# Kernel optimization log

Hardware: AMD Instinct MI355X
Metric: run time of the kernel (lower is better)

The kernel has to match this reference:

```python
import jax, jax.numpy as jnp
import numpy as np

B, T, V, E, D, F = 128, 64, 10000, 512, 512, 2048


def setup_inputs() -> dict:
    key = jax.random.key(0)
    ks = iter(jax.random.split(key, 40))
    def nrm(shape, s=0.02):
        return (jax.random.normal(next(ks), shape, jnp.float32) * s)
    inp = {
        "image_vectors": jax.random.normal(next(ks), (B, F), jnp.float32),
        "captions_ix": jax.random.randint(next(ks), (B, T), 0, V),
        "emb": nrm((V, E)),
        "W_init_h1": nrm((D, F)), "b_init_h1": jnp.zeros((D,), jnp.float32),
        "W_init_c1": nrm((D, F)), "b_init_c1": jnp.zeros((D,), jnp.float32),
        "W_init_h2": nrm((D, F)), "b_init_h2": jnp.zeros((D,), jnp.float32),
        "W_init_c2": nrm((D, F)), "b_init_c2": jnp.zeros((D,), jnp.float32),
        "W_ih1": nrm((4 * D, E)), "W_hh1": nrm((4 * D, D)), "b1": jnp.zeros((4 * D,), jnp.float32),
        "W_ih2": nrm((4 * D, 2 * D)), "W_hh2": nrm((4 * D, D)), "b2": jnp.zeros((4 * D,), jnp.float32),
        "Wv1": nrm((D, D)), "bv1": jnp.zeros((D,), jnp.float32),
        "Wo1": nrm((D, D)), "bo1": jnp.zeros((D,), jnp.float32),
        "Wv2": nrm((D, D)), "bv2": jnp.zeros((D,), jnp.float32),
        "Wo2": nrm((D, D)), "bo2": jnp.zeros((D,), jnp.float32),
        "W_logits": nrm((V, 3 * D)), "b_logits": jnp.zeros((V,), jnp.float32),
    }
    return inp


def _lstm(x, h0, c0, W_ih, W_hh, b):
    # x: [B,T,Din] -> hidden states [B,T,D]; PyTorch gate order (i,f,g,o), b = b_ih + b_hh.
    xp = jnp.einsum('btd,gd->btg', x, W_ih) + b  # precompute input projections
    def step(carry, xt):
        h, c = carry
        gates = xt + h @ W_hh.T
        i, f, g, o = jnp.split(gates, 4, axis=-1)
        c = jax.nn.sigmoid(f) * c + jax.nn.sigmoid(i) * jnp.tanh(g)
        h = jax.nn.sigmoid(o) * jnp.tanh(c)
        return (h, c), h
    _, hs = jax.lax.scan(step, (h0, c0), jnp.swapaxes(xp, 0, 1))
    return jnp.swapaxes(hs, 0, 1)


def reference(image_vectors, captions_ix, emb,
              W_init_h1, b_init_h1, W_init_c1, b_init_c1,
              W_init_h2, b_init_h2, W_init_c2, b_init_c2,
              W_ih1, W_hh1, b1, W_ih2, W_hh2, b2,
              Wv1, bv1, Wo1, bo1, Wv2, bv2, Wo2, bo2,
              W_logits, b_logits):
    h1 = image_vectors @ W_init_h1.T + b_init_h1
    c1 = image_vectors @ W_init_c1.T + b_init_c1
    h2 = image_vectors @ W_init_h2.T + b_init_h2
    c2 = image_vectors @ W_init_c2.T + b_init_c2
    x = emb[captions_ix]  # [B,T,E] (dropout p=0 -> identity)
    h1s = _lstm(x, h1, c1, W_ih1, W_hh1, b1)  # [B,T,D]; LSTM output == hidden state
    # MHA with key=value of length 1: softmax over one key is exactly 1, so the
    # output is out_proj(v_proj(key)) independent of the (growing prefix) query.
    attn1 = (h1s @ Wv1.T + bv1) @ Wo1.T + bo1  # [B,T,D]
    h2s = _lstm(jnp.concatenate([h1s, attn1], axis=-1), h2, c2, W_ih2, W_hh2, b2)
    attn2 = (h2s @ Wv2.T + bv2) @ Wo2.T + bo2
    out = jnp.concatenate([h2s, attn1, attn2], axis=-1)  # [B,T,3D]
    return out @ W_logits.T + b_logits  # [B,T,V]
```

## Files before the change

kernel.cpp:

```cpp
#include <hip/hip_runtime.h>
#include <stdint.h>

#define DEV __device__ __forceinline__

typedef short bf16x8 __attribute__((ext_vector_type(8)));
typedef float f32x4 __attribute__((ext_vector_type(4)));

DEV unsigned short f2bf(float f) {
  union { float f; uint32_t u; } v; v.f = f;
  return (unsigned short)((v.u + 0x7fffu + ((v.u >> 16) & 1u)) >> 16);
}
DEV float bf2f(unsigned short u) {
  union { uint32_t u; float f; } v; v.u = (uint32_t)u << 16; return v.f;
}

DEV float fsig(float x) { return 1.f / (1.f + __expf(-x)); }
DEV float ftanh(float x) { float e = __expf(2.f * x); return 1.f - 2.f / (e + 1.f); }

DEV void gload16(const void* g, void* lds) {
  __builtin_amdgcn_global_load_lds(
      (const __attribute__((address_space(1))) int*)(uintptr_t)g,
      (__attribute__((address_space(3))) int*)(uintptr_t)lds, 16, 0, 0);
}

template <int MODE>
__global__ __launch_bounds__(256) void gemm_nt(
    const unsigned short* __restrict__ A, int lda,
    const unsigned short* __restrict__ B, int ldb,
    void* __restrict__ P0, void* __restrict__ P1,
    void* __restrict__ P2, void* __restrict__ P3,
    int ldc, int ldc2,
    const float* __restrict__ bias,
    int K, int Nreal)
{
  __shared__ alignas(16) unsigned short Asm[128 * 32];
  __shared__ alignas(16) unsigned short Bsm[128 * 32];
  const int tid = threadIdx.x;
  const int wave = tid >> 6, lane = tid & 63;

  const int gx = gridDim.x;
  const int lin = blockIdx.y * gx + blockIdx.x;
  const int nwg = gx * gridDim.y;
  const int q = nwg >> 3, r = nwg & 7;
  const int xcd = lin & 7, i2 = lin >> 3;
  const int wg = (xcd < r ? xcd * (q + 1) : r * (q + 1) + (xcd - r) * q) + i2;
  const int m0 = (wg % gx) * 128, n0 = (wg / gx) * 128;

  const int wr = wave >> 1, wc = wave & 1;
  f32x4 acc[4][4] = {};

  const int q0 = tid, q1 = tid + 256;
  const unsigned short* Ag0 = A + (size_t)(m0 + (q0 >> 2)) * lda + (q0 & 3) * 8;
  const unsigned short* Ag1 = A + (size_t)(m0 + (q1 >> 2)) * lda + (q1 & 3) * 8;
  const unsigned short* Bg0 = B + (size_t)(n0 + (q0 >> 2)) * ldb + (q0 & 3) * 8;
  const unsigned short* Bg1 = B + (size_t)(n0 + (q1 >> 2)) * ldb + (q1 & 3) * 8;
  char* As0 = (char*)Asm + wave * 1024;  char* As1 = As0 + 4096;
  char* Bs0 = (char*)Bsm + wave * 1024;  char* Bs1 = Bs0 + 4096;

  const int ra = wr * 64 + (lane & 15);
  const int rb = wc * 64 + (lane & 15);
  const int kb = (lane >> 4) * 16;

  for (int k0 = 0; k0 < K; k0 += 32) {
    gload16(Ag0 + k0, As0);
    gload16(Ag1 + k0, As1);
    gload16(Bg0 + k0, Bs0);
    gload16(Bg1 + k0, Bs1);
    __syncthreads();
    bf16x8 af[4], bfr[4];
#pragma unroll
    for (int i = 0; i < 4; ++i)
      af[i] = *(const bf16x8*)((const char*)Asm + (ra + i * 16) * 64 + kb);
#pragma unroll
    for (int i = 0; i < 4; ++i)
      bfr[i] = *(const bf16x8*)((const char*)Bsm + (rb + i * 16) * 64 + kb);
#pragma unroll
    for (int mi = 0; mi < 4; ++mi)
#pragma unroll
      for (int ni = 0; ni < 4; ++ni)
        acc[mi][ni] = __builtin_amdgcn_mfma_f32_16x16x32_bf16(af[mi], bfr[ni], acc[mi][ni], 0, 0, 0);
    __syncthreads();
  }

  const int row0 = m0 + wr * 64 + (lane >> 4) * 4;
  const int col0 = n0 + wc * 64 + (lane & 15);

  if constexpr (MODE == 2) {
#pragma unroll
    for (int mi = 0; mi < 4; ++mi) {
      const int rowb = row0 + mi * 16;
      const int dd = rowb >> 2;
      const float4 b4 = *(const float4*)&bias[rowb];
#pragma unroll
      for (int ni = 0; ni < 4; ++ni) {
        const int col = col0 + ni * 16;
        const int tt = col & 63, bb = col >> 6;
        float4 v;
        v.x = acc[mi][ni][0] + b4.x;
        v.y = acc[mi][ni][1] + b4.y;
        v.z = acc[mi][ni][2] + b4.z;
        v.w = acc[mi][ni][3] + b4.w;
        const int wgid = (bb >> 4) * 16 + (dd >> 5);
        const int ww = (dd >> 3) & 3, mi2 = (dd >> 2) & 1, ln = (dd & 3) * 16 + (bb & 15);
        ((float4*)P0)[((((size_t)tt * 128 + wgid) * 4 + ww) * 2 + mi2) * 64 + ln] = v;
      }
    }
    return;
  }

#pragma unroll
  for (int mi = 0; mi < 4; ++mi) {
#pragma unroll
    for (int ni = 0; ni < 4; ++ni) {
      const int col = col0 + ni * 16;
      if (col >= Nreal) continue;
      const float bs = bias ? bias[col] : 0.f;
#pragma unroll
      for (int rr = 0; rr < 4; ++rr) {
        const int row = row0 + mi * 16 + rr;
        const float v = acc[mi][ni][rr] + bs;
        if constexpr (MODE == 1) {
          ((unsigned short*)P0)[(size_t)row * ldc + col] = f2bf(v);
          if (P1) ((unsigned short*)P1)[(size_t)row * ldc2 + col] = f2bf(v);
        } else if constexpr (MODE == 4) {
          const unsigned short ad = ((const unsigned short*)P1)[(size_t)row * ldc2 + col];
          ((unsigned short*)P0)[(size_t)row * ldc + col] = f2bf(v + bf2f(ad));
        } else {
          const int seg = col >> 9, cc = col & 511;
          if (seg == 0)      ((unsigned short*)P0)[(size_t)row * 512 + cc] = f2bf(v);
          else if (seg == 1) ((float*)P1)[(size_t)row * 512 + cc] = v;
          else if (seg == 2) ((unsigned short*)P2)[(size_t)row * 512 + cc] = f2bf(v);
          else               ((float*)P3)[(size_t)row * 512 + cc] = v;
        }
      }
    }
  }
}

__global__ __launch_bounds__(512, 2) void gemm256(
    const unsigned short* __restrict__ A, int lda,
    const unsigned short* __restrict__ B, int ldb,
    float* __restrict__ C, int ldc,
    const float* __restrict__ bias, int K, int Nreal)
{
  __shared__ alignas(16) unsigned short Lds[2][2][16384];
  const int tid = threadIdx.x;
  const int wave = tid >> 6, lane = tid & 63;
  const int fr = lane & 15, kq = lane >> 4;

  const int gx = gridDim.x;
  const int lin = blockIdx.y * gx + blockIdx.x;
  const int nwg = gx * gridDim.y;
  const int q8 = nwg >> 3, r8 = nwg & 7;
  const int xcd = lin & 7, i2 = lin >> 3;
  const int wg = (xcd < r8 ? xcd * (q8 + 1) : r8 * (q8 + 1) + (xcd - r8) * q8) + i2;
  const int m0 = (wg % gx) * 256, n0 = (wg / gx) * 256;

  const int wr = wave >> 2, wc = wave & 3;

  const unsigned short* srcA[4];
  const unsigned short* srcB[4];
  int dstO[4];
#pragma unroll
  for (int s = 0; s < 4; ++s) {
    const int c = tid + s * 512;
    const int row = c >> 3, qp = (c & 7) ^ (row & 7);
    srcA[s] = A + (size_t)(m0 + row) * lda + qp * 8;
    srcB[s] = B + (size_t)(n0 + row) * ldb + qp * 8;
    dstO[s] = (wave * 64 + s * 512) * 16;
  }

  const int NT = K >> 6;
#define STAGE256(kt, buf)                                            \
  {                                                                  \
    _Pragma("unroll")                                                \
    for (int s = 0; s < 4; ++s)                                      \
      gload16(srcA[s] + (kt) * 64, (char*)&Lds[buf][0][0] + dstO[s]);\
    _Pragma("unroll")                                                \
    for (int s = 0; s < 4; ++s)                                      \
      gload16(srcB[s] + (kt) * 64, (char*)&Lds[buf][1][0] + dstO[s]);\
  }
  STAGE256(0, 0);
  STAGE256(1, 1);

  f32x4 acc[8][4] = {};
  const int slot0 = (kq ^ (fr & 7)) * 16;

  for (int kt = 0; kt < NT; ++kt) {
    asm volatile("s_waitcnt vmcnt(8)" ::: "memory");
    __builtin_amdgcn_sched_barrier(0);
    __builtin_amdgcn_s_barrier();
    __builtin_amdgcn_sched_barrier(0);
    const char* bufA = (const char*)&Lds[kt & 1][0][0];
    const char* bufB = (const char*)&Lds[kt & 1][1][0];
    bf16x8 Bf[4][2];
#pragma unroll
    for (int n = 0; n < 4; ++n) {
      const char* bb = bufB + (wc * 64 + n * 16 + fr) * 128;
      Bf[n][0] = *(const bf16x8*)(bb + slot0);
      Bf[n][1] = *(const bf16x8*)(bb + (slot0 ^ 64));
    }
#pragma unroll
    for (int q = 0; q < 4; ++q) {
      bf16x8 Af[2][2];
#pragma unroll
      for (int m2 = 0; m2 < 2; ++m2) {
        const char* ab = bufA + (wr * 128 + q * 32 + m2 * 16 + fr) * 128;
        Af[m2][0] = *(const bf16x8*)(ab + slot0);
        Af[m2][1] = *(const bf16x8*)(ab + (slot0 ^ 64));
      }
      __builtin_amdgcn_s_setprio(1);
#pragma unroll
      for (int m2 = 0; m2 < 2; ++m2)
#pragma unroll
        for (int n = 0; n < 4; ++n) {
          acc[q * 2 + m2][n] = __builtin_amdgcn_mfma_f32_16x16x32_bf16(
              Af[m2][0], Bf[n][0], acc[q * 2 + m2][n], 0, 0, 0);
          acc[q * 2 + m2][n] = __builtin_amdgcn_mfma_f32_16x16x32_bf16(
              Af[m2][1], Bf[n][1], acc[q * 2 + m2][n], 0, 0, 0);
        }
      __builtin_amdgcn_s_setprio(0);
    }
    __builtin_amdgcn_sched_barrier(0);
    __builtin_amdgcn_s_barrier();
    __builtin_amdgcn_sched_barrier(0);
    const int kn = (kt + 2 < NT) ? kt + 2 : 0;
    STAGE256(kn, kt & 1);
  }

#pragma unroll
  for (int mf = 0; mf < 8; ++mf) {
    const int row = m0 + wr * 128 + mf * 16 + kq * 4;
#pragma unroll
    for (int n = 0; n < 4; ++n) {
      const int col = n0 + wc * 64 + n * 16 + fr;
      if (col < Nreal) {
        const float bs = bias[col];
#pragma unroll
        for (int rr = 0; rr < 4; ++rr)
          __builtin_nontemporal_store(acc[mf][n][rr] + bs,
                                      &C[(size_t)(row + rr) * ldc + col]);
      }
    }
  }
#undef STAGE256
}

__global__ __launch_bounds__(256, 1) void lstm_fused(
    const unsigned short* __restrict__ Whh1, const unsigned short* __restrict__ Whh2,
    const unsigned short* __restrict__ Weff2r,
    const unsigned short* __restrict__ h01, const unsigned short* __restrict__ h02,
    const float* __restrict__ c1st, const float* __restrict__ c2st,
    const float* __restrict__ xpr,
    const float* __restrict__ beff2,
    unsigned short* __restrict__ hx1, unsigned short* __restrict__ hx2,
    unsigned short* __restrict__ hcat,
    int* __restrict__ flags)
{
  __shared__ unsigned short Wsm[8][128][64];
  __shared__ uint32_t Hst[16][16];
  const int tid = threadIdx.x;
  const bool role2 = blockIdx.x >= 128;
  const int wg = role2 ? blockIdx.x - 128 : blockIdx.x;
  const int g = wg >> 4, s = wg & 15;
  const int w = tid >> 6, lane = tid & 63, fr = lane & 15, kq = lane >> 4;

  {
    const unsigned short* Whh = role2 ? Whh2 : Whh1;
    const int m = tid >> 1;
    const int row = (m & 3) * 512 + s * 32 + (m >> 2);
    const unsigned short* src = Whh + (size_t)row * 512 + (tid & 1) * 256;
#pragma unroll 4
    for (int cc = 0; cc < 32; ++cc) {
      const int k = (tid & 1) * 256 + cc * 8;
      uint4 v = *(const uint4*)(src + cc * 8);
      const int kblk = k >> 6, c = (k & 63) >> 3, sl = c ^ (m & 7);
      *(uint4*)((char*)&Wsm[kblk][m][0] + sl * 16) = v;
    }
  }

  const int b = g * 16 + fr;
  const int d0 = s * 32 + w * 8 + kq;
  const float* c0 = role2 ? c2st : c1st;
  float c_r[2];
  c_r[0] = c0[b * 512 + d0];
  c_r[1] = c0[b * 512 + d0 + 4];
  __syncthreads();

  int* fl1 = flags + g * 16;
  int* fl2 = flags + 128 + g * 16;
  int* flown = role2 ? fl2 : fl1;
  unsigned short* hxown = role2 ? hx2 : hx1;
  const unsigned short* hinit = role2 ? h02 : h01;
  const int colbase = (role2 ? 0 : 512) + s * 32;
  const float4* xv = (const float4*)xpr + ((size_t)(wg * 4 + w) * 2) * 64 + lane;
  float4 be0 = {0, 0, 0, 0}, be1 = {0, 0, 0, 0};
  if (role2) {
    be0 = *(const float4*)(beff2 + s * 128 + w * 32 + kq * 4);
    be1 = *(const float4*)(beff2 + s * 128 + w * 32 + 16 + kq * 4);
  }
  const size_t hxg = (size_t)g * 8192;

  for (int t = 0; t < 64; ++t) {
    f32x4 acc[2] = {};
    float4 xg0, xg1;

    if (!role2) {
      xg0 = xv[(size_t)t * 65536];
      xg1 = xv[(size_t)t * 65536 + 64];
      if (t) {
        if (w == 1) {
          for (;;) {
            bool ok = true;
            if (lane < 16)
              ok = __hip_atomic_load(fl1 + lane, __ATOMIC_RELAXED,
                                     __HIP_MEMORY_SCOPE_AGENT) >= t;
            if (__all(ok)) break;
            __builtin_amdgcn_s_sleep(1);
          }
        }
        __syncthreads();
      }
      bf16x8 hf[16];
      if (t == 0) {
#pragma unroll
        for (int kk = 0; kk < 16; ++kk)
          hf[kk] = *(const bf16x8*)(hinit + (size_t)b * 512 + kk * 32 + kq * 8);
      } else {
        const unsigned short* hb = hx1 + (size_t)(t - 1) * 65536 + hxg + fr * 32 + kq * 8;
#pragma unroll
        for (int kk = 0; kk < 16; ++kk)
          hf[kk] = *(const bf16x8*)(hb + kk * 512);
      }
#pragma unroll
      for (int kk = 0; kk < 16; ++kk) {
        const int kblk = kk >> 1, cbase = (kk & 1) * 4 + kq;
#pragma unroll
        for (int mi = 0; mi < 2; ++mi) {
          const int m = w * 32 + mi * 16 + fr;
          const int sl = cbase ^ (m & 7);
          const bf16x8 af = *(const bf16x8*)((const char*)&Wsm[kblk][m][0] + sl * 16);
          acc[mi] = __builtin_amdgcn_mfma_f32_16x16x32_bf16(af, hf[kk], acc[mi], 0, 0, 0);
        }
      }
    } else {
      xg0 = be0; xg1 = be1;
      if (w == 1) {
        for (;;) {
          bool ok = true;
          if (lane < 16)
            ok = __hip_atomic_load(fl1 + lane, __ATOMIC_RELAXED,
                                   __HIP_MEMORY_SCOPE_AGENT) >= t + 1;
          if (__all(ok)) break;
          __builtin_amdgcn_s_sleep(1);
        }
      }
      __syncthreads();
      {
        const unsigned short* h1b = hx1 + (size_t)t * 65536 + hxg + fr * 32 + kq * 8;
        bf16x8 hf1[16];
#pragma unroll
        for (int kk = 0; kk < 16; ++kk)
          hf1[kk] = *(const bf16x8*)(h1b + kk * 512);
        const bf16x8* wr = (const bf16x8*)Weff2r + (size_t)s * 32 * 256 + tid;
#pragma unroll
        for (int kk = 0; kk < 16; ++kk) {
#pragma unroll
          for (int mi = 0; mi < 2; ++mi) {
            const bf16x8 af = wr[(kk * 2 + mi) * 256];
            acc[mi] = __builtin_amdgcn_mfma_f32_16x16x32_bf16(af, hf1[kk], acc[mi], 0, 0, 0);
          }
        }
      }
      if (t) {
        if (w == 1) {
          for (;;) {
            bool ok = true;
            if (lane < 16)
              ok = __hip_atomic_load(fl2 + lane, __ATOMIC_RELAXED,
                                     __HIP_MEMORY_SCOPE_AGENT) >= t;
            if (__all(ok)) break;
            __builtin_amdgcn_s_sleep(1);
          }
        }
        __syncthreads();
      }
      bf16x8 hf[16];
      if (t == 0) {
#pragma unroll
        for (int kk = 0; kk < 16; ++kk)
          hf[kk] = *(const bf16x8*)(hinit + (size_t)b * 512 + kk * 32 + kq * 8);
      } else {
        const unsigned short* hb = hx2 + (size_t)(t - 1) * 65536 + hxg + fr * 32 + kq * 8;
#pragma unroll
        for (int kk = 0; kk < 16; ++kk)
          hf[kk] = *(const bf16x8*)(hb + kk * 512);
      }
#pragma unroll
      for (int kk = 0; kk < 16; ++kk) {
        const int kblk = kk >> 1, cbase = (kk & 1) * 4 + kq;
#pragma unroll
        for (int mi = 0; mi < 2; ++mi) {
          const int m = w * 32 + mi * 16 + fr;
          const int sl = cbase ^ (m & 7);
          const bf16x8 af = *(const bf16x8*)((const char*)&Wsm[kblk][m][0] + sl * 16);
          acc[mi] = __builtin_amdgcn_mfma_f32_16x16x32_bf16(af, hf[kk], acc[mi], 0, 0, 0);
        }
      }
    }

    unsigned short hn[2];
#pragma unroll
    for (int mi = 0; mi < 2; ++mi) {
      const float4 xg = mi ? xg1 : xg0;
      const float iv = acc[mi][0] + xg.x;
      const float fv = acc[mi][1] + xg.y;
      const float gv = acc[mi][2] + xg.z;
      const float ov = acc[mi][3] + xg.w;
      const float c = fsig(fv) * c_r[mi] + fsig(iv) * ftanh(gv);
      c_r[mi] = c;
      hn[mi] = f2bf(fsig(ov) * ftanh(c));
    }

    const uint32_t pk = (uint32_t)hn[0] | ((uint32_t)hn[1] << 16);
    const uint32_t y = (uint32_t)__shfl_xor((int)pk, 16);
    const uint32_t word = (kq & 1) ? __builtin_amdgcn_perm(pk, y, 0x07060302)
                                   : __builtin_amdgcn_perm(y, pk, 0x05040100);
    Hst[fr][w * 4 + ((kq & 1) ? 2 + (kq >> 1) : (kq >> 1))] = word;
    __syncthreads();

    if (w == 0) {
      const uint4 v = *(const uint4*)&Hst[lane >> 2][(lane & 3) * 4];
      unsigned short* dst = hxown + (size_t)t * 65536 + hxg + s * 512 + lane * 8;
      __hip_atomic_store((unsigned long long*)dst, ((const unsigned long long*)&v)[0],
                         __ATOMIC_RELAXED, __HIP_MEMORY_SCOPE_AGENT);
      __hip_atomic_store((unsigned long long*)(dst + 4), ((const unsigned long long*)&v)[1],
                         __ATOMIC_RELAXED, __HIP_MEMORY_SCOPE_AGENT);
      asm volatile("s_waitcnt vmcnt(0)" ::: "memory");
      if (lane == 0)
        __hip_atomic_store(flown + s, t + 1, __ATOMIC_RELAXED, __HIP_MEMORY_SCOPE_AGENT);
      const int row = (g * 16 + (lane >> 2)) * 64 + t;
      *(uint4*)(hcat + (size_t)row * 1024 + colbase + (lane & 3) * 8) = v;
    }
  }
}

struct CastJobs {
  const float* src[12];
  unsigned short* dst[12];
  long nreal4[12];
  long cum4[13];
  int n;
};

__global__ void cast_multi4(CastJobs J) {
  const long total = J.cum4[J.n];
  for (long i = (long)blockIdx.x * blockDim.x + threadIdx.x; i < total;
       i += (long)gridDim.x * blockDim.x) {
    int s = 0;
    while (i >= J.cum4[s + 1]) ++s;
    const long off = i - J.cum4[s];
    float4 v = {0.f, 0.f, 0.f, 0.f};
    if (off < J.nreal4[s]) v = ((const float4*)J.src[s])[off];
    ushort4 o;
    o.x = f2bf(v.x); o.y = f2bf(v.y); o.z = f2bf(v.z); o.w = f2bf(v.w);
    ((ushort4*)J.dst[s])[off] = o;
  }
}

__global__ void prep1(const float* __restrict__ Wv1, const float* __restrict__ Wv2,
                      const float* __restrict__ Wihl1, const float* __restrict__ Wihl2,
                      const float* __restrict__ b1, const float* __restrict__ b2,
                      const float* __restrict__ bih1, const float* __restrict__ bic1,
                      const float* __restrict__ bih2, const float* __restrict__ bic2,
                      const float* __restrict__ Wo1, const float* __restrict__ bv1,
                      const float* __restrict__ bo1,
                      const float* __restrict__ Wo2, const float* __restrict__ bv2,
                      const float* __restrict__ bo2,
                      unsigned short* __restrict__ WvT1, unsigned short* __restrict__ WvT2,
                      unsigned short* __restrict__ Wp1, unsigned short* __restrict__ Wp2,
                      float* __restrict__ bp1, float* __restrict__ bp2,
                      float* __restrict__ bcat,
                      float* __restrict__ bc1, float* __restrict__ bc2)
{
  const long NTOT = 924672;
  for (long id = (long)blockIdx.x * blockDim.x + threadIdx.x; id < NTOT;
       id += (long)gridDim.x * blockDim.x) {
    if (id < 131072) {
      const int m = (int)(id >> 6), kb = (int)(id & 63) * 8;
      const float* sp = Wihl1 + (size_t)((m & 3) * 512 + (m >> 2)) * 512 + kb;
      unsigned short o[8];
#pragma unroll
      for (int e = 0; e < 8; ++e) o[e] = f2bf(sp[e]);
      *(uint4*)(Wp1 + (size_t)m * 512 + kb) = *(const uint4*)o;
    } else if (id < 393216) {
      const long j = id - 131072;
      const int m = (int)(j >> 7), kb = (int)(j & 127) * 8;
      const float* sp = Wihl2 + (size_t)((m & 3) * 512 + (m >> 2)) * 1024 + kb;
      unsigned short o[8];
#pragma unroll
      for (int e = 0; e < 8; ++e) o[e] = f2bf(sp[e]);
      *(uint4*)(Wp2 + (size_t)m * 1024 + kb) = *(const uint4*)o;
    } else if (id < 917504) {
      const long t = id - 393216;
      const int which = (int)(t >> 18);
      const int u = (int)(t & 262143), a = u >> 9, bb = u & 511;
      (which ? WvT2 : WvT1)[u] = f2bf((which ? Wv2 : Wv1)[(size_t)bb * 512 + a]);
    } else if (id < 921600) {
      const int t = (int)(id - 917504);
      if (t < 2048) bp1[t] = b1[(t & 3) * 512 + (t >> 2)];
      else { const int m = t - 2048; bp2[m] = b2[(m & 3) * 512 + (m >> 2)]; }
    } else if (id < 923648) {
      const int i = (int)(id - 921600);
      const float* sarr[4] = {bih1, bic1, bih2, bic2};
      bcat[i] = sarr[i >> 9][i & 511];
    } else {
      const int i = (int)(id - 923648);
      const float* Wo = (i >= 512) ? Wo2 : Wo1;
      const float* bv = (i >= 512) ? bv2 : bv1;
      const float* bo = (i >= 512) ? bo2 : bo1;
      float* bc = (i >= 512) ? bc2 : bc1;
      const int r = i & 511;
      float sacc = bo[r];
      for (int k = 0; k < 512; k += 4) {
        const float4 wv = *(const float4*)(Wo + (size_t)r * 512 + k);
        const float4 bb = *(const float4*)(bv + k);
        sacc += wv.x * bb.x + wv.y * bb.y + wv.z * bb.z + wv.w * bb.w;
      }
      bc[r] = sacc;
    }
  }
}

__global__ void gather_rows(const int* __restrict__ ix, const float* __restrict__ emb,
                            unsigned short* __restrict__ x) {
  const int row = blockIdx.x;
  const int e = ix[row];
  const float4* s = (const float4*)(emb + (size_t)e * 512) + threadIdx.x * 2;
  const float4 a = s[0], b = s[1];
  unsigned short o[8] = {f2bf(a.x), f2bf(a.y), f2bf(a.z), f2bf(a.w),
                         f2bf(b.x), f2bf(b.y), f2bf(b.z), f2bf(b.w)};
  *(uint4*)(x + (size_t)row * 512 + threadIdx.x * 8) = *(const uint4*)o;
}

__global__ void reorder_wbf(const unsigned short* __restrict__ W,
                            unsigned short* __restrict__ R) {
  const int id = blockIdx.x * blockDim.x + threadIdx.x;
  const int tid = id & 255, mi = (id >> 8) & 1, kk = (id >> 9) & 15, s = id >> 13;
  const int w = tid >> 6, lane = tid & 63, fr = lane & 15, kq = lane >> 4;
  const int row = s * 128 + w * 32 + mi * 16 + fr;
  const int col = kk * 32 + kq * 8;
  *((uint4*)R + id) = *(const uint4*)(W + (size_t)row * 512 + col);
}

__global__ void bias2(const unsigned short* __restrict__ Wl, const float* __restrict__ blog,
                      const unsigned short* __restrict__ Wp2, const float* __restrict__ bp2,
                      const float* __restrict__ bc1, const float* __restrict__ bc2,
                      float* __restrict__ blcat, float* __restrict__ beff2) {
  const int lane = threadIdx.x & 63;
  if (blockIdx.x < 512) {
    const int m = blockIdx.x * 4 + (threadIdx.x >> 6);
    const unsigned short* row = Wp2 + (size_t)m * 1024 + 512;
    float sum = 0.f;
    for (int k = lane; k < 512; k += 64) sum += bf2f(row[k]) * bc1[k];
#pragma unroll
    for (int mm = 32; mm; mm >>= 1) sum += __shfl_xor(sum, mm, 64);
    if (lane == 0) beff2[m] = bp2[m] + sum;
  } else {
    const int j = (blockIdx.x - 512) * 4 + (threadIdx.x >> 6);
    const unsigned short* row = Wl + (size_t)j * 1536;
    float sum = 0.f;
    for (int k = lane; k < 512; k += 64) {
      sum += bf2f(row[512 + k]) * bc1[k];
      sum += bf2f(row[1024 + k]) * bc2[k];
    }
#pragma unroll
    for (int mm = 32; mm; mm >>= 1) sum += __shfl_xor(sum, mm, 64);
    if (lane == 0) blcat[j] = blog[j] + sum;
  }
}

extern "C" void kernel_launch(void* const* d_in, const int* in_sizes, int n_in,
                              void* d_out, int out_size, void* d_ws, size_t ws_size,
                              hipStream_t stream) {
  (void)in_sizes; (void)n_in; (void)out_size; (void)ws_size;
  const float* img    = (const float*)d_in[0];
  const int*   ix     = (const int*)d_in[1];
  const float* emb    = (const float*)d_in[2];
  const float* Wih1f  = (const float*)d_in[3];
  const float* bih1   = (const float*)d_in[4];
  const float* Wic1f  = (const float*)d_in[5];
  const float* bic1   = (const float*)d_in[6];
  const float* Wih2f  = (const float*)d_in[7];
  const float* bih2   = (const float*)d_in[8];
  const float* Wic2f  = (const float*)d_in[9];
  const float* bic2   = (const float*)d_in[10];
  const float* Wihl1  = (const float*)d_in[11];
  const float* Whhl1  = (const float*)d_in[12];
  const float* b1     = (const float*)d_in[13];
  const float* Wihl2  = (const float*)d_in[14];
  const float* Whhl2  = (const float*)d_in[15];
  const float* b2     = (const float*)d_in[16];
  const float* Wv1    = (const float*)d_in[17];
  const float* bv1    = (const float*)d_in[18];
  const float* Wo1    = (const float*)d_in[19];
  const float* bo1    = (const float*)d_in[20];
  const float* Wv2    = (const float*)d_in[21];
  const float* bv2    = (const float*)d_in[22];
  const float* Wo2    = (const float*)d_in[23];
  const float* bo2    = (const float*)d_in[24];
  const float* Wlog   = (const float*)d_in[25];
  const float* blog   = (const float*)d_in[26];
  float* out = (float*)d_out;

  char* p = (char*)d_ws;
  auto al = [&](size_t bytes) { char* r = p; p += (bytes + 255) & ~(size_t)255; return r; };
  unsigned short* Wp1    = (unsigned short*)al((size_t)2048 * 512 * 2);
  unsigned short* Whh1_b = (unsigned short*)al((size_t)2048 * 512 * 2);
  unsigned short* Wp2    = (unsigned short*)al((size_t)2048 * 1024 * 2);
  unsigned short* Whh2_b = (unsigned short*)al((size_t)2048 * 512 * 2);
  unsigned short* WvT1   = (unsigned short*)al((size_t)512 * 512 * 2);
  unsigned short* Wo1_b  = (unsigned short*)al((size_t)512 * 512 * 2);
  unsigned short* WvT2   = (unsigned short*)al((size_t)512 * 512 * 2);
  unsigned short* Wo2_b  = (unsigned short*)al((size_t)512 * 512 * 2);
  unsigned short* Wc1T   = (unsigned short*)al((size_t)512 * 512 * 2);
  unsigned short* Wc2T   = (unsigned short*)al((size_t)512 * 512 * 2);
  unsigned short* Wlog_b = (unsigned short*)al((size_t)10240 * 1536 * 2);
  unsigned short* Wcat   = (unsigned short*)al((size_t)10240 * 1024 * 2);
  unsigned short* Weff2  = (unsigned short*)al((size_t)2048 * 512 * 2);
  unsigned short* Weff2r = (unsigned short*)al((size_t)2048 * 512 * 2);
  unsigned short* Wh1i_b = (unsigned short*)al((size_t)512 * 2048 * 2);
  unsigned short* Wc1i_b = (unsigned short*)al((size_t)512 * 2048 * 2);
  unsigned short* Wh2i_b = (unsigned short*)al((size_t)512 * 2048 * 2);
  unsigned short* Wc2i_b = (unsigned short*)al((size_t)512 * 2048 * 2);
  unsigned short* img_b  = (unsigned short*)al((size_t)128 * 2048 * 2);
  unsigned short* x_b    = (unsigned short*)al((size_t)8192 * 512 * 2);
  float*          xpr    = (float*)al((size_t)8192 * 2048 * 4);
  unsigned short* hcat   = (unsigned short*)al((size_t)8192 * 1024 * 2);
  unsigned short* hx1    = (unsigned short*)al((size_t)64 * 128 * 512 * 2);
  unsigned short* hx2    = (unsigned short*)al((size_t)64 * 128 * 512 * 2);
  unsigned short* h01    = (unsigned short*)al((size_t)128 * 512 * 2);
  unsigned short* h02    = (unsigned short*)al((size_t)128 * 512 * 2);
  float*          c1st   = (float*)al((size_t)128 * 512 * 4);
  float*          c2st   = (float*)al((size_t)128 * 512 * 4);
  float*          bcat   = (float*)al((size_t)2048 * 4);
  float*          bp1    = (float*)al((size_t)2048 * 4);
  float*          bp2    = (float*)al((size_t)2048 * 4);
  float*          bc1    = (float*)al((size_t)512 * 4);
  float*          bc2    = (float*)al((size_t)512 * 4);
  float*          beff2  = (float*)al((size_t)2048 * 4);
  float*          blcat  = (float*)al((size_t)10240 * 4);
  int*            flags  = (int*)al(2048);

  hipMemsetAsync(flags, 0, 2048, stream);

  CastJobs J = {};
  auto addjob = [&](const float* s, unsigned short* d, long nreal, long ntot) {
    J.src[J.n] = s; J.dst[J.n] = d; J.nreal4[J.n] = nreal / 4;
    J.cum4[J.n + 1] = J.cum4[J.n] + ntot / 4; ++J.n;
  };
  addjob(img,   img_b,  (long)128 * 2048,   (long)128 * 2048);
  addjob(Whhl1, Whh1_b, (long)2048 * 512,   (long)2048 * 512);
  addjob(Whhl2, Whh2_b, (long)2048 * 512,   (long)2048 * 512);
  addjob(Wo1,   Wo1_b,  (long)512 * 512,    (long)512 * 512);
  addjob(Wo2,   Wo2_b,  (long)512 * 512,    (long)512 * 512);
  addjob(Wih1f, Wh1i_b, (long)512 * 2048,   (long)512 * 2048);
  addjob(Wic1f, Wc1i_b, (long)512 * 2048,   (long)512 * 2048);
  addjob(Wih2f, Wh2i_b, (long)512 * 2048,   (long)512 * 2048);
  addjob(Wic2f, Wc2i_b, (long)512 * 2048,   (long)512 * 2048);
  addjob(Wlog,  Wlog_b, (long)10000 * 1536, (long)10240 * 1536);
  cast_multi4<<<2048, 256, 0, stream>>>(J);

  prep1<<<1024, 256, 0, stream>>>(Wv1, Wv2, Wihl1, Wihl2, b1, b2,
                                  bih1, bic1, bih2, bic2,
                                  Wo1, bv1, bo1, Wo2, bv2, bo2,
                                  WvT1, WvT2, Wp1, Wp2, bp1, bp2, bcat, bc1, bc2);

  gather_rows<<<8192, 64, 0, stream>>>(ix, emb, x_b);

  gemm_nt<1><<<dim3(4, 4), 256, 0, stream>>>(
      WvT1, 512, Wo1_b, 512, Wc1T, nullptr, nullptr, nullptr, 512, 0, nullptr, 512, 512);
  gemm_nt<1><<<dim3(4, 4), 256, 0, stream>>>(
      WvT2, 512, Wo2_b, 512, Wc2T, nullptr, nullptr, nullptr, 512, 0, nullptr, 512, 512);

  gemm_nt<4><<<dim3(16, 4), 256, 0, stream>>>(
      Wp2 + 512, 1024, Wc1T, 512, Weff2, Wp2, nullptr, nullptr, 512, 1024, nullptr, 512, 512);
  reorder_wbf<<<512, 256, 0, stream>>>(Weff2, Weff2r);
  bias2<<<3012, 256, 0, stream>>>(Wlog_b, blog, Wp2, bp2, bc1, bc2, blcat, beff2);

  gemm_nt<4><<<dim3(80, 4), 256, 0, stream>>>(
      Wlog_b + 1024, 1536, Wc2T, 512, Wcat, Wlog_b, nullptr, nullptr, 1024, 1536,
      nullptr, 512, 512);
  gemm_nt<1><<<dim3(80, 4), 256, 0, stream>>>(
      Wlog_b + 512, 1536, Wc1T, 512, Wcat + 512, nullptr, nullptr, nullptr, 1024, 0,
      nullptr, 512, 512);

  gemm_nt<3><<<dim3(1, 16), 256, 0, stream>>>(
      img_b, 2048, Wh1i_b, 2048, h01, c1st, h02, c2st, 0, 0, bcat, 2048, 2048);

  gemm_nt<2><<<dim3(16, 64), 256, 0, stream>>>(
      Wp1, 512, x_b, 512, xpr, nullptr, nullptr, nullptr, 0, 0, bp1, 512, 8192);

  lstm_fused<<<256, 256, 0, stream>>>(
      Whh1_b, Whh2_b, Weff2r, h01, h02, c1st, c2st, xpr, beff2, hx1, hx2, hcat, flags);

  gemm256<<<dim3(32, 40), 512, 0, stream>>>(
      hcat, 1024, Wcat, 1024, out, 10000, blcat, 1024, 10000);
}
```

Baseline: 838.3 us.

## Fuse LSTM1 input projection into recurrent kernel and relax step synchronization

Drops the separate x@Wp1 GEMM and its 64 MB fp32 xpr buffer. Each layer-1 workgroup now computes its input-projection MFMAs from the bf16 embeddings and a reordered Wp1 copy read from global memory, before waiting on the previous step's hidden state, so that work can overlap the wait. The recurrent h exchange no longer stages through LDS; each wave writes its packed words straight to the hx buffers. Waiting is done per half of the K dimension on flag subsets by all waves, which removes the single-wave poll followed by a barrier. In exchange there are more scattered 4-byte global stores and extra weight reads on every timestep inside the serial critical path.

```diff
diff --git a/kernel.cpp b/kernel.cpp
--- a/kernel.cpp
+++ b/kernel.cpp
@@ -84,29 +84,6 @@
 
   const int row0 = m0 + wr * 64 + (lane >> 4) * 4;
   const int col0 = n0 + wc * 64 + (lane & 15);
-
-  if constexpr (MODE == 2) {
-#pragma unroll
-    for (int mi = 0; mi < 4; ++mi) {
-      const int rowb = row0 + mi * 16;
-      const int dd = rowb >> 2;
-      const float4 b4 = *(const float4*)&bias[rowb];
-#pragma unroll
-      for (int ni = 0; ni < 4; ++ni) {
-        const int col = col0 + ni * 16;
-        const int tt = col & 63, bb = col >> 6;
-        float4 v;
-        v.x = acc[mi][ni][0] + b4.x;
-        v.y = acc[mi][ni][1] + b4.y;
-        v.z = acc[mi][ni][2] + b4.z;
-        v.w = acc[mi][ni][3] + b4.w;
-        const int wgid = (bb >> 4) * 16 + (dd >> 5);
-        const int ww = (dd >> 3) & 3, mi2 = (dd >> 2) & 1, ln = (dd & 3) * 16 + (bb & 15);
-        ((float4*)P0)[((((size_t)tt * 128 + wgid) * 4 + ww) * 2 + mi2) * 64 + ln] = v;
-      }
-    }
-    return;
-  }
 
 #pragma unroll
   for (int mi = 0; mi < 4; ++mi) {
@@ -248,17 +225,18 @@
 
 __global__ __launch_bounds__(256, 1) void lstm_fused(
     const unsigned short* __restrict__ Whh1, const unsigned short* __restrict__ Whh2,
+    const unsigned short* __restrict__ Wp1r,
     const unsigned short* __restrict__ Weff2r,
+    const unsigned short* __restrict__ x_b,
     const unsigned short* __restrict__ h01, const unsigned short* __restrict__ h02,
     const float* __restrict__ c1st, const float* __restrict__ c2st,
-    const float* __restrict__ xpr,
+    const float* __restrict__ bp1,
     const float* __restrict__ beff2,
     unsigned short* __restrict__ hx1, unsigned short* __restrict__ hx2,
     unsigned short* __restrict__ hcat,
     int* __restrict__ flags)
 {
   __shared__ unsigned short Wsm[8][128][64];
-  __shared__ uint32_t Hst[16][16];
   const int tid = threadIdx.x;
   const bool role2 = blockIdx.x >= 128;
   const int wg = role2 ? blockIdx.x - 128 : blockIdx.x;
@@ -291,128 +269,106 @@
   int* fl2 = flags + 128 + g * 16;
   int* flown = role2 ? fl2 : fl1;
   unsigned short* hxown = role2 ? hx2 : hx1;
+  const unsigned short* hxsrcA = role2 ? hx2 : hx1;
   const unsigned short* hinit = role2 ? h02 : h01;
   const int colbase = (role2 ? 0 : 512) + s * 32;
-  const float4* xv = (const float4*)xpr + ((size_t)(wg * 4 + w) * 2) * 64 + lane;
-  float4 be0 = {0, 0, 0, 0}, be1 = {0, 0, 0, 0};
-  if (role2) {
-    be0 = *(const float4*)(beff2 + s * 128 + w * 32 + kq * 4);
-    be1 = *(const float4*)(beff2 + s * 128 + w * 32 + 16 + kq * 4);
-  }
+  const float* bsrc = role2 ? beff2 : bp1;
+  const float4 be0 = *(const float4*)(bsrc + s * 128 + w * 32 + kq * 4);
+  const float4 be1 = *(const float4*)(bsrc + s * 128 + w * 32 + 16 + kq * 4);
+  const bf16x8* wrB = (const bf16x8*)(role2 ? Weff2r : Wp1r) + (size_t)s * 32 * 256 + tid;
   const size_t hxg = (size_t)g * 8192;
+  const int pos2 = (kq & 1) ? 2 + (kq >> 1) : (kq >> 1);
 
   for (int t = 0; t < 64; ++t) {
     f32x4 acc[2] = {};
-    float4 xg0, xg1;
 
     if (!role2) {
-      xg0 = xv[(size_t)t * 65536];
-      xg1 = xv[(size_t)t * 65536 + 64];
-      if (t) {
-        if (w == 1) {
-          for (;;) {
-            bool ok = true;
-            if (lane < 16)
-              ok = __hip_atomic_load(fl1 + lane, __ATOMIC_RELAXED,
-                                     __HIP_MEMORY_SCOPE_AGENT) >= t;
-            if (__all(ok)) break;
-            __builtin_amdgcn_s_sleep(1);
-          }
-        }
-        __syncthreads();
-      }
+      const unsigned short* xb = x_b + ((size_t)b * 64 + t) * 512 + kq * 8;
+      bf16x8 xf[16];
+#pragma unroll
+      for (int kk = 0; kk < 16; ++kk)
+        xf[kk] = *(const bf16x8*)(xb + kk * 32);
+#pragma unroll
+      for (int kk = 0; kk < 16; ++kk) {
+#pragma unroll
+        for (int mi = 0; mi < 2; ++mi)
+          acc[mi] = __builtin_amdgcn_mfma_f32_16x16x32_bf16(
+              wrB[(kk * 2 + mi) * 256], xf[kk], acc[mi], 0, 0, 0);
+      }
+    } else {
+      for (;;) {
+        bool ok = true;
+        if (lane < 16)
+          ok = __hip_atomic_load(fl1 + lane, __ATOMIC_RELAXED,
+                                 __HIP_MEMORY_SCOPE_AGENT) >= t + 1;
+        if (__all(ok)) break;
+        __builtin_amdgcn_s_sleep(1);
+      }
+      const unsigned short* h1b = hx1 + (size_t)t * 65536 + hxg + fr * 32 + kq * 8;
+      bf16x8 hf1[16];
+#pragma unroll
+      for (int kk = 0; kk < 16; ++kk)
+        hf1[kk] = *(const bf16x8*)(h1b + kk * 512);
+#pragma unroll
+      for (int kk = 0; kk < 16; ++kk) {
+#pragma unroll
+        for (int mi = 0; mi < 2; ++mi)
+          acc[mi] = __builtin_amdgcn_mfma_f32_16x16x32_bf16(
+              wrB[(kk * 2 + mi) * 256], hf1[kk], acc[mi], 0, 0, 0);
+      }
+    }
+
+    if (t == 0) {
       bf16x8 hf[16];
-      if (t == 0) {
-#pragma unroll
-        for (int kk = 0; kk < 16; ++kk)
-          hf[kk] = *(const bf16x8*)(hinit + (size_t)b * 512 + kk * 32 + kq * 8);
-      } else {
-        const unsigned short* hb = hx1 + (size_t)(t - 1) * 65536 + hxg + fr * 32 + kq * 8;
-#pragma unroll
-        for (int kk = 0; kk < 16; ++kk)
-          hf[kk] = *(const bf16x8*)(hb + kk * 512);
-      }
+#pragma unroll
+      for (int kk = 0; kk < 16; ++kk)
+        hf[kk] = *(const bf16x8*)(hinit + (size_t)b * 512 + kk * 32 + kq * 8);
 #pragma unroll
       for (int kk = 0; kk < 16; ++kk) {
         const int kblk = kk >> 1, cbase = (kk & 1) * 4 + kq;
 #pragma unroll
         for (int mi = 0; mi < 2; ++mi) {
           const int m = w * 32 + mi * 16 + fr;
-          const int sl = cbase ^ (m & 7);
-          const bf16x8 af = *(const bf16x8*)((const char*)&Wsm[kblk][m][0] + sl * 16);
+          const bf16x8 af = *(const bf16x8*)((const char*)&Wsm[kblk][m][0] +
+                                             (cbase ^ (m & 7)) * 16);
           acc[mi] = __builtin_amdgcn_mfma_f32_16x16x32_bf16(af, hf[kk], acc[mi], 0, 0, 0);
         }
       }
     } else {
-      xg0 = be0; xg1 = be1;
-      if (w == 1) {
+      const unsigned short* hb = hxsrcA + (size_t)(t - 1) * 65536 + hxg + fr * 32 + kq * 8;
+#pragma unroll
+      for (int half = 0; half < 2; ++half) {
         for (;;) {
           bool ok = true;
-          if (lane < 16)
-            ok = __hip_atomic_load(fl1 + lane, __ATOMIC_RELAXED,
-                                   __HIP_MEMORY_SCOPE_AGENT) >= t + 1;
+          if (lane < 8)
+            ok = __hip_atomic_load(flown + half * 8 + lane, __ATOMIC_RELAXED,
+                                   __HIP_MEMORY_SCOPE_AGENT) >= t;
           if (__all(ok)) break;
           __builtin_amdgcn_s_sleep(1);
         }
-      }
-      __syncthreads();
-      {
-        const unsigned short* h1b = hx1 + (size_t)t * 65536 + hxg + fr * 32 + kq * 8;
-        bf16x8 hf1[16];
-#pragma unroll
-        for (int kk = 0; kk < 16; ++kk)
-          hf1[kk] = *(const bf16x8*)(h1b + kk * 512);
-        const bf16x8* wr = (const bf16x8*)Weff2r + (size_t)s * 32 * 256 + tid;
-#pragma unroll
-        for (int kk = 0; kk < 16; ++kk) {
+        bf16x8 hf[8];
+#pragma unroll
+        for (int k2 = 0; k2 < 8; ++k2)
+          hf[k2] = *(const bf16x8*)(hb + (half * 8 + k2) * 512);
+#pragma unroll
+        for (int k2 = 0; k2 < 8; ++k2) {
+          const int kk = half * 8 + k2;
+          const int kblk = kk >> 1, cbase = (kk & 1) * 4 + kq;
 #pragma unroll
           for (int mi = 0; mi < 2; ++mi) {
-            const bf16x8 af = wr[(kk * 2 + mi) * 256];
-            acc[mi] = __builtin_amdgcn_mfma_f32_16x16x32_bf16(af, hf1[kk], acc[mi], 0, 0, 0);
+            const int m = w * 32 + mi * 16 + fr;
+            const bf16x8 af = *(const bf16x8*)((const char*)&Wsm[kblk][m][0] +
+                                               (cbase ^ (m & 7)) * 16);
+            acc[mi] = __builtin_amdgcn_mfma_f32_16x16x32_bf16(af, hf[k2], acc[mi], 0, 0, 0);
           }
         }
       }
-      if (t) {
-        if (w == 1) {
-          for (;;) {
-            bool ok = true;
-            if (lane < 16)
-              ok = __hip_atomic_load(fl2 + lane, __ATOMIC_RELAXED,
-                                     __HIP_MEMORY_SCOPE_AGENT) >= t;
-            if (__all(ok)) break;
-            __builtin_amdgcn_s_sleep(1);
-          }
-        }
-        __syncthreads();
-      }
-      bf16x8 hf[16];
-      if (t == 0) {
-#pragma unroll
-        for (int kk = 0; kk < 16; ++kk)
-          hf[kk] = *(const bf16x8*)(hinit + (size_t)b * 512 + kk * 32 + kq * 8);
-      } else {
-        const unsigned short* hb = hx2 + (size_t)(t - 1) * 65536 + hxg + fr * 32 + kq * 8;
-#pragma unroll
-        for (int kk = 0; kk < 16; ++kk)
-          hf[kk] = *(const bf16x8*)(hb + kk * 512);
-      }
-#pragma unroll
-      for (int kk = 0; kk < 16; ++kk) {
-        const int kblk = kk >> 1, cbase = (kk & 1) * 4 + kq;
-#pragma unroll
-        for (int mi = 0; mi < 2; ++mi) {
-          const int m = w * 32 + mi * 16 + fr;
-          const int sl = cbase ^ (m & 7);
-          const bf16x8 af = *(const bf16x8*)((const char*)&Wsm[kblk][m][0] + sl * 16);
-          acc[mi] = __builtin_amdgcn_mfma_f32_16x16x32_bf16(af, hf[kk], acc[mi], 0, 0, 0);
-        }
-      }
     }
 
     unsigned short hn[2];
 #pragma unroll
     for (int mi = 0; mi < 2; ++mi) {
-      const float4 xg = mi ? xg1 : xg0;
+      const float4 xg = mi ? be1 : be0;
       const float iv = acc[mi][0] + xg.x;
       const float fv = acc[mi][1] + xg.y;
       const float gv = acc[mi][2] + xg.z;
@@ -426,22 +382,13 @@
     const uint32_t y = (uint32_t)__shfl_xor((int)pk, 16);
     const uint32_t word = (kq & 1) ? __builtin_amdgcn_perm(pk, y, 0x07060302)
                                    : __builtin_amdgcn_perm(y, pk, 0x05040100);
-    Hst[fr][w * 4 + ((kq & 1) ? 2 + (kq >> 1) : (kq >> 1))] = word;
+    unsigned short* dst = hxown + (size_t)t * 65536 + hxg + s * 512 + fr * 32 + w * 8 + pos2 * 2;
+    __hip_atomic_store((uint32_t*)dst, word, __ATOMIC_RELAXED, __HIP_MEMORY_SCOPE_AGENT);
+    asm volatile("s_waitcnt vmcnt(0)" ::: "memory");
     __syncthreads();
-
-    if (w == 0) {
-      const uint4 v = *(const uint4*)&Hst[lane >> 2][(lane & 3) * 4];
-      unsigned short* dst = hxown + (size_t)t * 65536 + hxg + s * 512 + lane * 8;
-      __hip_atomic_store((unsigned long long*)dst, ((const unsigned long long*)&v)[0],
-                         __ATOMIC_RELAXED, __HIP_MEMORY_SCOPE_AGENT);
-      __hip_atomic_store((unsigned long long*)(dst + 4), ((const unsigned long long*)&v)[1],
-                         __ATOMIC_RELAXED, __HIP_MEMORY_SCOPE_AGENT);
-      asm volatile("s_waitcnt vmcnt(0)" ::: "memory");
-      if (lane == 0)
-        __hip_atomic_store(flown + s, t + 1, __ATOMIC_RELAXED, __HIP_MEMORY_SCOPE_AGENT);
-      const int row = (g * 16 + (lane >> 2)) * 64 + t;
-      *(uint4*)(hcat + (size_t)row * 1024 + colbase + (lane & 3) * 8) = v;
-    }
+    if (tid == 0)
+      __hip_atomic_store(flown + s, t + 1, __ATOMIC_RELAXED, __HIP_MEMORY_SCOPE_AGENT);
+    *(uint32_t*)(hcat + ((size_t)(g * 16 + fr) * 64 + t) * 1024 + colbase + w * 8 + pos2 * 2) = word;
   }
 }
 
@@ -543,14 +490,19 @@
   *(uint4*)(x + (size_t)row * 512 + threadIdx.x * 8) = *(const uint4*)o;
 }
 
-__global__ void reorder_wbf(const unsigned short* __restrict__ W,
-                            unsigned short* __restrict__ R) {
+__global__ void reorder_wbf2(const unsigned short* __restrict__ WA,
+                             const unsigned short* __restrict__ WB,
+                             unsigned short* __restrict__ RA,
+                             unsigned short* __restrict__ RB) {
   const int id = blockIdx.x * blockDim.x + threadIdx.x;
-  const int tid = id & 255, mi = (id >> 8) & 1, kk = (id >> 9) & 15, s = id >> 13;
+  const unsigned short* W = (id >= 131072) ? WB : WA;
+  unsigned short* R = (id >= 131072) ? RB : RA;
+  const int t = id & 131071;
+  const int tid = t & 255, mi = (t >> 8) & 1, kk = (t >> 9) & 15, s = t >> 13;
   const int w = tid >> 6, lane = tid & 63, fr = lane & 15, kq = lane >> 4;
   const int row = s * 128 + w * 32 + mi * 16 + fr;
   const int col = kk * 32 + kq * 8;
-  *((uint4*)R + id) = *(const uint4*)(W + (size_t)row * 512 + col);
+  *((uint4*)R + t) = *(const uint4*)(W + (size_t)row * 512 + col);
 }
 
 __global__ void bias2(const unsigned short* __restrict__ Wl, const float* __restrict__ blog,
@@ -616,6 +568,7 @@
   char* p = (char*)d_ws;
   auto al = [&](size_t bytes) { char* r = p; p += (bytes + 255) & ~(size_t)255; return r; };
   unsigned short* Wp1    = (unsigned short*)al((size_t)2048 * 512 * 2);
+  unsigned short* Wp1r   = (unsigned short*)al((size_t)2048 * 512 * 2);
   unsigned short* Whh1_b = (unsigned short*)al((size_t)2048 * 512 * 2);
   unsigned short* Wp2    = (unsigned short*)al((size_t)2048 * 1024 * 2);
   unsigned short* Whh2_b = (unsigned short*)al((size_t)2048 * 512 * 2);
@@ -635,7 +588,6 @@
   unsigned short* Wc2i_b = (unsigned short*)al((size_t)512 * 2048 * 2);
   unsigned short* img_b  = (unsigned short*)al((size_t)128 * 2048 * 2);
   unsigned short* x_b    = (unsigned short*)al((size_t)8192 * 512 * 2);
-  float*          xpr    = (float*)al((size_t)8192 * 2048 * 4);
   unsigned short* hcat   = (unsigned short*)al((size_t)8192 * 1024 * 2);
   unsigned short* hx1    = (unsigned short*)al((size_t)64 * 128 * 512 * 2);
   unsigned short* hx2    = (unsigned short*)al((size_t)64 * 128 * 512 * 2);
@@ -685,7 +637,7 @@
 
   gemm_nt<4><<<dim3(16, 4), 256, 0, stream>>>(
       Wp2 + 512, 1024, Wc1T, 512, Weff2, Wp2, nullptr, nullptr, 512, 1024, nullptr, 512, 512);
-  reorder_wbf<<<512, 256, 0, stream>>>(Weff2, Weff2r);
+  reorder_wbf2<<<1024, 256, 0, stream>>>(Wp1, Weff2, Wp1r, Weff2r);
   bias2<<<3012, 256, 0, stream>>>(Wlog_b, blog, Wp2, bp2, bc1, bc2, blcat, beff2);
 
   gemm_nt<4><<<dim3(80, 4), 256, 0, stream>>>(
@@ -698,11 +650,9 @@
   gemm_nt<3><<<dim3(1, 16), 256, 0, stream>>>(
       img_b, 2048, Wh1i_b, 2048, h01, c1st, h02, c2st, 0, 0, bcat, 2048, 2048);
 
-  gemm_nt<2><<<dim3(16, 64), 256, 0, stream>>>(
-      Wp1, 512, x_b, 512, xpr, nullptr, nullptr, nullptr, 0, 0, bp1, 512, 8192);
-
   lstm_fused<<<256, 256, 0, stream>>>(
-      Whh1_b, Whh2_b, Weff2r, h01, h02, c1st, c2st, xpr, beff2, hx1, hx2, hcat, flags);
+      Whh1_b, Whh2_b, Wp1r, Weff2r, x_b, h01, h02, c1st, c2st,
+      bp1, beff2, hx1, hx2, hcat, flags);
 
   gemm256<<<dim3(32, 40), 512, 0, stream>>>(
       hcat, 1024, Wcat, 1024, out, 10000, blcat, 1024, 10000);
```

New measurement: 968.2 us. 1.15x slower.
